# Optimization experiments

Hardware: AMD Instinct MI355X
Metric: run time of the kernel (lower is better)

Reference implementation:

```python
import jax, jax.numpy as jnp
import numpy as np


def setup_inputs() -> dict:
    key = jax.random.key(0)
    k1, k2 = jax.random.split(key)
    B, T, D, K = 16, 800, 256, 64
    x = jax.random.normal(k1, (B, T, D), dtype=jnp.float32)
    mu = jax.random.normal(k2, (K, D), dtype=jnp.float32)
    prec = jnp.ones((K,), dtype=jnp.float32)
    return {"x": x, "mu": mu, "prec": prec}


def reference(x, mu, prec):
    # x: (B,T,D), mu: (K,D), prec: (K,)
    delta = x[:, :, None, :] - mu[None, None, :, :]          # (B,T,K,D)
    dist = jnp.sum(delta * delta, axis=-1)                   # (B,T,K) dist_pow=2
    llk = -(prec * prec) * dist                              # use_bias=False -> bias=0
    r = jax.nn.softmax(llk, axis=-1)                         # softmax over components K
    r = r / (jnp.sum(r, axis=1, keepdims=True) + 1e-9)       # normalize over time T
    pool = jnp.einsum('btk,btkd->bkd', r, delta)             # weighted sum over T
    return pool.reshape(x.shape[0], -1)                      # (B, K*D)
```

## Files before the change

kernel.cpp:

```cpp
#include <hip/hip_runtime.h>

#define B_ 16
#define T_ 800
#define D_ 256
#define K_ 64
#define NTILE 13

__global__ __launch_bounds__(512, 1) void kernelAB(
    const float* __restrict__ x, const float* __restrict__ mu,
    const float* __restrict__ prec, float* __restrict__ Pp, float* __restrict__ Spart)
{
    __shared__ float xs[64 * 260];
    __shared__ float mus[64 * 260];
    __shared__ float rt[64 * 68];
    __shared__ float xxs[64];
    __shared__ float mms[64];
    __shared__ float sred[8][64];

    const int tid  = threadIdx.x;
    const int tx   = tid >> 4;
    const int ky   = tid & 15;
    const int b    = blockIdx.x / NTILE;
    const int tile = blockIdx.x % NTILE;
    const int t0   = tile * 64;

    #pragma unroll
    for (int jj = 0; jj < 8; ++jj) {
        const int g   = tid + jj * 512;
        const int row = g >> 6, col = g & 63;
        int trow = t0 + row; if (trow > T_ - 1) trow = T_ - 1;
        *(float4*)&xs[row * 260 + col * 4] =
            *(const float4*)(x + ((size_t)(b * T_ + trow)) * D_ + col * 4);
        *(float4*)&mus[row * 260 + col * 4] =
            *(const float4*)(mu + (size_t)row * D_ + col * 4);
    }
    __syncthreads();

    {
        const int srow = tid >> 3, sq = tid & 7;
        float xxp = 0.f, mmp = 0.f;
        #pragma unroll
        for (int m = 0; m < 8; ++m) {
            float4 v = *(const float4*)&xs[srow * 260 + (sq * 8 + m) * 4];
            xxp = fmaf(v.x, v.x, xxp); xxp = fmaf(v.y, v.y, xxp);
            xxp = fmaf(v.z, v.z, xxp); xxp = fmaf(v.w, v.w, xxp);
            float4 u = *(const float4*)&mus[srow * 260 + (sq * 8 + m) * 4];
            mmp = fmaf(u.x, u.x, mmp); mmp = fmaf(u.y, u.y, mmp);
            mmp = fmaf(u.z, u.z, mmp); mmp = fmaf(u.w, u.w, mmp);
        }
        xxp += __shfl_xor(xxp, 1); xxp += __shfl_xor(xxp, 2); xxp += __shfl_xor(xxp, 4);
        mmp += __shfl_xor(mmp, 1); mmp += __shfl_xor(mmp, 2); mmp += __shfl_xor(mmp, 4);
        if (sq == 0) { xxs[srow] = xxp; mms[srow] = mmp; }
    }
    __syncthreads();

    float acc[2][4];
    #pragma unroll
    for (int i = 0; i < 2; ++i)
        #pragma unroll
        for (int j = 0; j < 4; ++j) acc[i][j] = 0.f;

    #pragma unroll 4
    for (int dg = 0; dg < 64; ++dg) {
        float4 xv[2], mv[4];
        #pragma unroll
        for (int i = 0; i < 2; ++i) xv[i] = *(const float4*)&xs[(tx * 2 + i) * 260 + dg * 4];
        #pragma unroll
        for (int j = 0; j < 4; ++j) mv[j] = *(const float4*)&mus[(ky + 16 * j) * 260 + dg * 4];
        #pragma unroll
        for (int i = 0; i < 2; ++i)
            #pragma unroll
            for (int j = 0; j < 4; ++j) {
                float a = acc[i][j];
                a = fmaf(xv[i].x, mv[j].x, a);
                a = fmaf(xv[i].y, mv[j].y, a);
                a = fmaf(xv[i].z, mv[j].z, a);
                a = fmaf(xv[i].w, mv[j].w, a);
                acc[i][j] = a;
            }
    }

    float p2[4], mmk[4];
    #pragma unroll
    for (int j = 0; j < 4; ++j) {
        float p = prec[ky + 16 * j];
        p2[j] = p * p;
        mmk[j] = mms[ky + 16 * j];
    }

    float sacc[4] = {0.f, 0.f, 0.f, 0.f};
    #pragma unroll
    for (int i = 0; i < 2; ++i) {
        const int tl = tx * 2 + i;
        const bool valid = (t0 + tl) < T_;
        const float xxv = xxs[tl];
        float llk[4];
        #pragma unroll
        for (int j = 0; j < 4; ++j)
            llk[j] = p2[j] * (2.f * acc[i][j] - xxv - mmk[j]);
        float mx = fmaxf(fmaxf(llk[0], llk[1]), fmaxf(llk[2], llk[3]));
        mx = fmaxf(mx, __shfl_xor(mx, 1)); mx = fmaxf(mx, __shfl_xor(mx, 2));
        mx = fmaxf(mx, __shfl_xor(mx, 4)); mx = fmaxf(mx, __shfl_xor(mx, 8));
        float e[4], ps = 0.f;
        #pragma unroll
        for (int j = 0; j < 4; ++j) { e[j] = __expf(llk[j] - mx); ps += e[j]; }
        ps += __shfl_xor(ps, 1); ps += __shfl_xor(ps, 2);
        ps += __shfl_xor(ps, 4); ps += __shfl_xor(ps, 8);
        const float inv = valid ? (1.f / ps) : 0.f;
        float4 rv;
        rv.x = e[0] * inv; rv.y = e[1] * inv; rv.z = e[2] * inv; rv.w = e[3] * inv;
        *(float4*)&rt[tl * 68 + ky * 4] = rv;
        sacc[0] += rv.x; sacc[1] += rv.y; sacc[2] += rv.z; sacc[3] += rv.w;
    }

    #pragma unroll
    for (int j = 0; j < 4; ++j) {
        sacc[j] += __shfl_xor(sacc[j], 16);
        sacc[j] += __shfl_xor(sacc[j], 32);
    }
    const int w = tid >> 6;
    if ((tid & 48) == 0) {
        #pragma unroll
        for (int j = 0; j < 4; ++j) sred[w][ky * 4 + j] = sacc[j];
    }
    __syncthreads();
    if (tid < 64) {
        const int k = tid;
        const int slot = (k & 15) * 4 + (k >> 4);
        float s = 0.f;
        #pragma unroll
        for (int q = 0; q < 8; ++q) s += sred[q][slot];
        Spart[((size_t)b * NTILE + tile) * K_ + k] = s;
    }

    const int dhalf = tid & 31;
    const int kx2   = tid >> 5;

    float4 pa[4][2];
    #pragma unroll
    for (int j = 0; j < 4; ++j) {
        pa[j][0] = make_float4(0.f, 0.f, 0.f, 0.f);
        pa[j][1] = make_float4(0.f, 0.f, 0.f, 0.f);
    }

    #pragma unroll 8
    for (int tt = 0; tt < 64; ++tt) {
        const float4 rv  = *(const float4*)&rt[tt * 68 + kx2 * 4];
        const float4 xv0 = *(const float4*)&xs[tt * 260 + dhalf * 4];
        const float4 xv1 = *(const float4*)&xs[tt * 260 + 128 + dhalf * 4];
        #pragma unroll
        for (int j = 0; j < 4; ++j) {
            const float rj = (j == 0) ? rv.x : (j == 1) ? rv.y : (j == 2) ? rv.z : rv.w;
            pa[j][0].x = fmaf(rj, xv0.x, pa[j][0].x);
            pa[j][0].y = fmaf(rj, xv0.y, pa[j][0].y);
            pa[j][0].z = fmaf(rj, xv0.z, pa[j][0].z);
            pa[j][0].w = fmaf(rj, xv0.w, pa[j][0].w);
            pa[j][1].x = fmaf(rj, xv1.x, pa[j][1].x);
            pa[j][1].y = fmaf(rj, xv1.y, pa[j][1].y);
            pa[j][1].z = fmaf(rj, xv1.z, pa[j][1].z);
            pa[j][1].w = fmaf(rj, xv1.w, pa[j][1].w);
        }
    }

    float* Pb = Pp + ((size_t)(b * NTILE + tile)) * K_ * D_;
    #pragma unroll
    for (int j = 0; j < 4; ++j) {
        const int k = kx2 + 16 * j;
        float* dst = Pb + (size_t)k * D_ + dhalf * 4;
        *(float4*)(dst)       = pa[j][0];
        *(float4*)(dst + 128) = pa[j][1];
    }
}

__global__ __launch_bounds__(256) void kernelC(
    const float* __restrict__ Pp, const float* __restrict__ Spart,
    const float* __restrict__ mu, float* __restrict__ out)
{
    const int o4 = blockIdx.x * 256 + threadIdx.x;
    const int d4 = o4 & 63;
    const int k  = (o4 >> 6) & 63;
    const int b  = o4 >> 12;

    float s = 0.f;
    #pragma unroll
    for (int p = 0; p < NTILE; ++p)
        s += Spart[((size_t)b * NTILE + p) * K_ + k];

    float4 acc = make_float4(0.f, 0.f, 0.f, 0.f);
    #pragma unroll
    for (int p = 0; p < NTILE; ++p) {
        float4 v = ((const float4*)Pp)[((size_t)(b * NTILE + p) * K_ + k) * (D_ / 4) + d4];
        acc.x += v.x; acc.y += v.y; acc.z += v.z; acc.w += v.w;
    }
    const float inv = 1.f / (s + 1e-9f);
    const float sm  = s * inv;
    const float4 m = ((const float4*)mu)[k * 64 + d4];
    float4 o;
    o.x = acc.x * inv - sm * m.x;
    o.y = acc.y * inv - sm * m.y;
    o.z = acc.z * inv - sm * m.z;
    o.w = acc.w * inv - sm * m.w;
    ((float4*)out)[o4] = o;
}

extern "C" void kernel_launch(void* const* d_in, const int* in_sizes, int n_in,
                              void* d_out, int out_size, void* d_ws, size_t ws_size,
                              hipStream_t stream) {
    const float* x    = (const float*)d_in[0];
    const float* mu   = (const float*)d_in[1];
    const float* prec = (const float*)d_in[2];
    float* out = (float*)d_out;

    float* Pp    = (float*)d_ws;
    float* Spart = Pp + (size_t)B_ * NTILE * K_ * D_;

    kernelAB<<<B_ * NTILE, 512, 0, stream>>>(x, mu, prec, Pp, Spart);
    kernelC<<<256, 256, 0, stream>>>(Pp, Spart, mu, out);
}
```

Measured before the change: 85.01 us.

## Use split-bf16 MFMA for distance and pooling GEMMs, precompute norms in prep kernel

Both matmuls in kernelAB (x·mu for distances and r^T·x for pooling) move from scalar FP32 FMAs to bf16 MFMA 16x16x32 instructions. fp32 precision is emulated by splitting operands into hi/lo bf16 parts: three products for the distance GEMM, and for pooling the responsibilities are rounded to bf16 while x keeps its hi/lo split. A new prep kernel precomputes the squared norms of x and mu and prec^2 in global memory. The block shrinks to 256 threads, and x is transposed into an XOR-swizzled shared layout for the second GEMM. This adds an extra launch and a full read of x, and the bf16 rounding of r may cost accuracy.

```diff
diff --git a/kernel.cpp b/kernel.cpp
--- a/kernel.cpp
+++ b/kernel.cpp
@@ -6,169 +6,213 @@
 #define K_ 64
 #define NTILE 13
 
-__global__ __launch_bounds__(512, 1) void kernelAB(
+typedef __attribute__((ext_vector_type(8))) short short8v;
+typedef __attribute__((ext_vector_type(4))) float f32x4v;
+
+__device__ __forceinline__ ushort bf16rn(float v) {
+    unsigned int b = __float_as_uint(v);
+    return (ushort)((b + 0x7fffu + ((b >> 16) & 1u)) >> 16);
+}
+__device__ __forceinline__ float bf16hi(ushort h) {
+    return __uint_as_float(((unsigned int)h) << 16);
+}
+
+__global__ __launch_bounds__(256) void prep(
+    const float* __restrict__ x, const float* __restrict__ mu, const float* __restrict__ prec,
+    float* __restrict__ xx_g, float* __restrict__ mm_g, float* __restrict__ p2_g)
+{
+    const int bid = blockIdx.x, tid = threadIdx.x;
+    if (bid < 3200) {
+        const int row = bid * 4 + (tid >> 6), lane = tid & 63;
+        float4 v = ((const float4*)x)[(size_t)row * 64 + lane];
+        float s = v.x*v.x + v.y*v.y + v.z*v.z + v.w*v.w;
+        #pragma unroll
+        for (int off = 32; off > 0; off >>= 1) s += __shfl_xor(s, off);
+        if (lane == 0) xx_g[row] = s;
+    } else if (bid < 3216) {
+        const int row = (bid - 3200) * 4 + (tid >> 6), lane = tid & 63;
+        float4 v = ((const float4*)mu)[(size_t)row * 64 + lane];
+        float s = v.x*v.x + v.y*v.y + v.z*v.z + v.w*v.w;
+        #pragma unroll
+        for (int off = 32; off > 0; off >>= 1) s += __shfl_xor(s, off);
+        if (lane == 0) mm_g[row] = s;
+    } else {
+        if (tid < 64) { float p = prec[tid]; p2_g[tid] = p * p; }
+    }
+}
+
+__global__ __launch_bounds__(256, 1) void kernelAB(
     const float* __restrict__ x, const float* __restrict__ mu,
-    const float* __restrict__ prec, float* __restrict__ Pp, float* __restrict__ Spart)
+    const float* __restrict__ xx_g, const float* __restrict__ mm_g,
+    const float* __restrict__ p2_g,
+    float* __restrict__ Pp, float* __restrict__ Spart)
 {
-    __shared__ float xs[64 * 260];
-    __shared__ float mus[64 * 260];
-    __shared__ float rt[64 * 68];
-    __shared__ float xxs[64];
-    __shared__ float mms[64];
-    __shared__ float sred[8][64];
+    __shared__ ushort xh_s[64 * 264];
+    __shared__ ushort xl_s[64 * 264];
+    __shared__ ushort muh_s[64 * 264];
+    __shared__ ushort mul_s[64 * 264];
+    __shared__ ushort rtT_s[64 * 72];
+    __shared__ float xxs[64], mms[64], p2s[64];
+    __shared__ float sred[4][64];
 
     const int tid  = threadIdx.x;
-    const int tx   = tid >> 4;
-    const int ky   = tid & 15;
+    const int lane = tid & 63;
+    const int w    = tid >> 6;
+    const int m    = lane & 15;
+    const int q    = lane >> 4;
     const int b    = blockIdx.x / NTILE;
     const int tile = blockIdx.x % NTILE;
     const int t0   = tile * 64;
 
-    #pragma unroll
-    for (int jj = 0; jj < 8; ++jj) {
-        const int g   = tid + jj * 512;
-        const int row = g >> 6, col = g & 63;
+    if (tid < 64)       xxs[tid]       = xx_g[b * T_ + min(t0 + tid, T_ - 1)];
+    else if (tid < 128) mms[tid - 64]  = mm_g[tid - 64];
+    else if (tid < 192) p2s[tid - 128] = p2_g[tid - 128];
+
+    #pragma unroll 4
+    for (int jj = 0; jj < 16; ++jj) {
+        const int idx = tid + jj * 256;
+        const int row = idx >> 6, c = idx & 63;
         int trow = t0 + row; if (trow > T_ - 1) trow = T_ - 1;
-        *(float4*)&xs[row * 260 + col * 4] =
-            *(const float4*)(x + ((size_t)(b * T_ + trow)) * D_ + col * 4);
-        *(float4*)&mus[row * 260 + col * 4] =
-            *(const float4*)(mu + (size_t)row * D_ + col * 4);
+        float4 v = ((const float4*)x)[(size_t)(b * T_ + trow) * 64 + c];
+        ushort4 h, l;
+        h.x = bf16rn(v.x); l.x = bf16rn(v.x - bf16hi(h.x));
+        h.y = bf16rn(v.y); l.y = bf16rn(v.y - bf16hi(h.y));
+        h.z = bf16rn(v.z); l.z = bf16rn(v.z - bf16hi(h.z));
+        h.w = bf16rn(v.w); l.w = bf16rn(v.w - bf16hi(h.w));
+        *(ushort4*)&xh_s[row * 264 + c * 4] = h;
+        *(ushort4*)&xl_s[row * 264 + c * 4] = l;
+    }
+    #pragma unroll 4
+    for (int jj = 0; jj < 16; ++jj) {
+        const int idx = tid + jj * 256;
+        const int row = idx >> 6, c = idx & 63;
+        float4 v = ((const float4*)mu)[(size_t)row * 64 + c];
+        ushort4 h, l;
+        h.x = bf16rn(v.x); l.x = bf16rn(v.x - bf16hi(h.x));
+        h.y = bf16rn(v.y); l.y = bf16rn(v.y - bf16hi(h.y));
+        h.z = bf16rn(v.z); l.z = bf16rn(v.z - bf16hi(h.z));
+        h.w = bf16rn(v.w); l.w = bf16rn(v.w - bf16hi(h.w));
+        *(ushort4*)&muh_s[row * 264 + c * 4] = h;
+        *(ushort4*)&mul_s[row * 264 + c * 4] = l;
     }
     __syncthreads();
 
-    {
-        const int srow = tid >> 3, sq = tid & 7;
-        float xxp = 0.f, mmp = 0.f;
-        #pragma unroll
-        for (int m = 0; m < 8; ++m) {
-            float4 v = *(const float4*)&xs[srow * 260 + (sq * 8 + m) * 4];
-            xxp = fmaf(v.x, v.x, xxp); xxp = fmaf(v.y, v.y, xxp);
-            xxp = fmaf(v.z, v.z, xxp); xxp = fmaf(v.w, v.w, xxp);
-            float4 u = *(const float4*)&mus[srow * 260 + (sq * 8 + m) * 4];
-            mmp = fmaf(u.x, u.x, mmp); mmp = fmaf(u.y, u.y, mmp);
-            mmp = fmaf(u.z, u.z, mmp); mmp = fmaf(u.w, u.w, mmp);
-        }
-        xxp += __shfl_xor(xxp, 1); xxp += __shfl_xor(xxp, 2); xxp += __shfl_xor(xxp, 4);
-        mmp += __shfl_xor(mmp, 1); mmp += __shfl_xor(mmp, 2); mmp += __shfl_xor(mmp, 4);
-        if (sq == 0) { xxs[srow] = xxp; mms[srow] = mmp; }
-    }
-    __syncthreads();
-
-    float acc[2][4];
-    #pragma unroll
-    for (int i = 0; i < 2; ++i)
-        #pragma unroll
-        for (int j = 0; j < 4; ++j) acc[i][j] = 0.f;
-
-    #pragma unroll 4
-    for (int dg = 0; dg < 64; ++dg) {
-        float4 xv[2], mv[4];
-        #pragma unroll
-        for (int i = 0; i < 2; ++i) xv[i] = *(const float4*)&xs[(tx * 2 + i) * 260 + dg * 4];
-        #pragma unroll
-        for (int j = 0; j < 4; ++j) mv[j] = *(const float4*)&mus[(ky + 16 * j) * 260 + dg * 4];
-        #pragma unroll
-        for (int i = 0; i < 2; ++i)
-            #pragma unroll
-            for (int j = 0; j < 4; ++j) {
-                float a = acc[i][j];
-                a = fmaf(xv[i].x, mv[j].x, a);
-                a = fmaf(xv[i].y, mv[j].y, a);
-                a = fmaf(xv[i].z, mv[j].z, a);
-                a = fmaf(xv[i].w, mv[j].w, a);
-                acc[i][j] = a;
-            }
-    }
-
-    float p2[4], mmk[4];
-    #pragma unroll
-    for (int j = 0; j < 4; ++j) {
-        float p = prec[ky + 16 * j];
-        p2[j] = p * p;
-        mmk[j] = mms[ky + 16 * j];
-    }
-
+    f32x4v acc[4];
+    #pragma unroll
+    for (int nt = 0; nt < 4; ++nt) acc[nt] = (f32x4v){0.f, 0.f, 0.f, 0.f};
+
+    #pragma unroll 2
+    for (int c = 0; c < 8; ++c) {
+        const int ao = (w * 16 + m) * 264 + c * 32 + q * 8;
+        short8v ah = *(const short8v*)&xh_s[ao];
+        short8v al = *(const short8v*)&xl_s[ao];
+        #pragma unroll
+        for (int nt = 0; nt < 4; ++nt) {
+            const int bo = (nt * 16 + m) * 264 + c * 32 + q * 8;
+            short8v bh = *(const short8v*)&muh_s[bo];
+            short8v bl = *(const short8v*)&mul_s[bo];
+            acc[nt] = __builtin_amdgcn_mfma_f32_16x16x32_bf16(ah, bh, acc[nt], 0, 0, 0);
+            acc[nt] = __builtin_amdgcn_mfma_f32_16x16x32_bf16(ah, bl, acc[nt], 0, 0, 0);
+            acc[nt] = __builtin_amdgcn_mfma_f32_16x16x32_bf16(al, bh, acc[nt], 0, 0, 0);
+        }
+    }
+
+    float mmk[4], p2k[4];
+    #pragma unroll
+    for (int nt = 0; nt < 4; ++nt) { mmk[nt] = mms[nt * 16 + m]; p2k[nt] = p2s[nt * 16 + m]; }
+
+    ushort4 rp[4];
     float sacc[4] = {0.f, 0.f, 0.f, 0.f};
     #pragma unroll
-    for (int i = 0; i < 2; ++i) {
-        const int tl = tx * 2 + i;
+    for (int r = 0; r < 4; ++r) {
+        const int tl = w * 16 + q * 4 + r;
+        const float xxv = xxs[tl];
         const bool valid = (t0 + tl) < T_;
-        const float xxv = xxs[tl];
         float llk[4];
         #pragma unroll
-        for (int j = 0; j < 4; ++j)
-            llk[j] = p2[j] * (2.f * acc[i][j] - xxv - mmk[j]);
+        for (int nt = 0; nt < 4; ++nt)
+            llk[nt] = p2k[nt] * (2.f * acc[nt][r] - xxv - mmk[nt]);
         float mx = fmaxf(fmaxf(llk[0], llk[1]), fmaxf(llk[2], llk[3]));
         mx = fmaxf(mx, __shfl_xor(mx, 1)); mx = fmaxf(mx, __shfl_xor(mx, 2));
         mx = fmaxf(mx, __shfl_xor(mx, 4)); mx = fmaxf(mx, __shfl_xor(mx, 8));
         float e[4], ps = 0.f;
         #pragma unroll
-        for (int j = 0; j < 4; ++j) { e[j] = __expf(llk[j] - mx); ps += e[j]; }
+        for (int nt = 0; nt < 4; ++nt) { e[nt] = __expf(llk[nt] - mx); ps += e[nt]; }
         ps += __shfl_xor(ps, 1); ps += __shfl_xor(ps, 2);
         ps += __shfl_xor(ps, 4); ps += __shfl_xor(ps, 8);
         const float inv = valid ? (1.f / ps) : 0.f;
-        float4 rv;
-        rv.x = e[0] * inv; rv.y = e[1] * inv; rv.z = e[2] * inv; rv.w = e[3] * inv;
-        *(float4*)&rt[tl * 68 + ky * 4] = rv;
-        sacc[0] += rv.x; sacc[1] += rv.y; sacc[2] += rv.z; sacc[3] += rv.w;
-    }
-
-    #pragma unroll
-    for (int j = 0; j < 4; ++j) {
-        sacc[j] += __shfl_xor(sacc[j], 16);
-        sacc[j] += __shfl_xor(sacc[j], 32);
-    }
-    const int w = tid >> 6;
-    if ((tid & 48) == 0) {
-        #pragma unroll
-        for (int j = 0; j < 4; ++j) sred[w][ky * 4 + j] = sacc[j];
+        #pragma unroll
+        for (int nt = 0; nt < 4; ++nt) {
+            float rv = e[nt] * inv;
+            sacc[nt] += rv;
+            ((ushort*)&rp[nt])[r] = bf16rn(rv);
+        }
+    }
+    #pragma unroll
+    for (int nt = 0; nt < 4; ++nt)
+        *(ushort4*)&rtT_s[(nt * 16 + m) * 72 + w * 16 + q * 4] = rp[nt];
+    #pragma unroll
+    for (int nt = 0; nt < 4; ++nt) {
+        sacc[nt] += __shfl_xor(sacc[nt], 16);
+        sacc[nt] += __shfl_xor(sacc[nt], 32);
+    }
+    if (q == 0) {
+        #pragma unroll
+        for (int nt = 0; nt < 4; ++nt) sred[w][nt * 16 + m] = sacc[nt];
     }
     __syncthreads();
+
     if (tid < 64) {
-        const int k = tid;
-        const int slot = (k & 15) * 4 + (k >> 4);
-        float s = 0.f;
-        #pragma unroll
-        for (int q = 0; q < 8; ++q) s += sred[q][slot];
-        Spart[((size_t)b * NTILE + tile) * K_ + k] = s;
-    }
-
-    const int dhalf = tid & 31;
-    const int kx2   = tid >> 5;
-
-    float4 pa[4][2];
-    #pragma unroll
-    for (int j = 0; j < 4; ++j) {
-        pa[j][0] = make_float4(0.f, 0.f, 0.f, 0.f);
-        pa[j][1] = make_float4(0.f, 0.f, 0.f, 0.f);
-    }
-
-    #pragma unroll 8
-    for (int tt = 0; tt < 64; ++tt) {
-        const float4 rv  = *(const float4*)&rt[tt * 68 + kx2 * 4];
-        const float4 xv0 = *(const float4*)&xs[tt * 260 + dhalf * 4];
-        const float4 xv1 = *(const float4*)&xs[tt * 260 + 128 + dhalf * 4];
-        #pragma unroll
-        for (int j = 0; j < 4; ++j) {
-            const float rj = (j == 0) ? rv.x : (j == 1) ? rv.y : (j == 2) ? rv.z : rv.w;
-            pa[j][0].x = fmaf(rj, xv0.x, pa[j][0].x);
-            pa[j][0].y = fmaf(rj, xv0.y, pa[j][0].y);
-            pa[j][0].z = fmaf(rj, xv0.z, pa[j][0].z);
-            pa[j][0].w = fmaf(rj, xv0.w, pa[j][0].w);
-            pa[j][1].x = fmaf(rj, xv1.x, pa[j][1].x);
-            pa[j][1].y = fmaf(rj, xv1.y, pa[j][1].y);
-            pa[j][1].z = fmaf(rj, xv1.z, pa[j][1].z);
-            pa[j][1].w = fmaf(rj, xv1.w, pa[j][1].w);
+        float s = sred[0][tid] + sred[1][tid] + sred[2][tid] + sred[3][tid];
+        Spart[((size_t)b * NTILE + tile) * K_ + tid] = s;
+    }
+
+    {
+        const int tp = tid & 31, dg = tid >> 5;
+        #pragma unroll
+        for (int c = 0; c < 4; ++c) {
+            short8v a0 = *(const short8v*)&xh_s[(2 * tp)     * 264 + dg * 32 + c * 8];
+            short8v a1 = *(const short8v*)&xh_s[(2 * tp + 1) * 264 + dg * 32 + c * 8];
+            short8v b0 = *(const short8v*)&xl_s[(2 * tp)     * 264 + dg * 32 + c * 8];
+            short8v b1 = *(const short8v*)&xl_s[(2 * tp + 1) * 264 + dg * 32 + c * 8];
+            #pragma unroll
+            for (int j = 0; j < 8; ++j) {
+                const int d = dg * 32 + c * 8 + j;
+                const int widx = (tp & 3) + 4 * ((tp >> 2) ^ (d & 7));
+                ushort2 hv, lv;
+                hv.x = (ushort)a0[j]; hv.y = (ushort)a1[j];
+                lv.x = (ushort)b0[j]; lv.y = (ushort)b1[j];
+                *(ushort2*)&muh_s[d * 64 + widx * 2] = hv;
+                *(ushort2*)&mul_s[d * 64 + widx * 2] = lv;
+            }
+        }
+    }
+    __syncthreads();
+
+    f32x4v acc2[16];
+    #pragma unroll
+    for (int nt = 0; nt < 16; ++nt) acc2[nt] = (f32x4v){0.f, 0.f, 0.f, 0.f};
+
+    #pragma unroll
+    for (int tc = 0; tc < 2; ++tc) {
+        short8v ar = *(const short8v*)&rtT_s[(w * 16 + m) * 72 + tc * 32 + q * 8];
+        #pragma unroll
+        for (int nt = 0; nt < 16; ++nt) {
+            const int drow = nt * 16 + m;
+            const int eoff = ((tc * 4 + q) ^ (drow & 7)) * 8;
+            short8v bh = *(const short8v*)&muh_s[drow * 64 + eoff];
+            short8v bl = *(const short8v*)&mul_s[drow * 64 + eoff];
+            acc2[nt] = __builtin_amdgcn_mfma_f32_16x16x32_bf16(ar, bh, acc2[nt], 0, 0, 0);
+            acc2[nt] = __builtin_amdgcn_mfma_f32_16x16x32_bf16(ar, bl, acc2[nt], 0, 0, 0);
         }
     }
 
     float* Pb = Pp + ((size_t)(b * NTILE + tile)) * K_ * D_;
     #pragma unroll
-    for (int j = 0; j < 4; ++j) {
-        const int k = kx2 + 16 * j;
-        float* dst = Pb + (size_t)k * D_ + dhalf * 4;
-        *(float4*)(dst)       = pa[j][0];
-        *(float4*)(dst + 128) = pa[j][1];
+    for (int nt = 0; nt < 16; ++nt) {
+        #pragma unroll
+        for (int r = 0; r < 4; ++r)
+            Pb[(size_t)(w * 16 + q * 4 + r) * D_ + nt * 16 + m] = acc2[nt][r];
     }
 }
 
@@ -213,7 +257,11 @@
 
     float* Pp    = (float*)d_ws;
     float* Spart = Pp + (size_t)B_ * NTILE * K_ * D_;
-
-    kernelAB<<<B_ * NTILE, 512, 0, stream>>>(x, mu, prec, Pp, Spart);
+    float* xx_g  = Spart + (size_t)B_ * NTILE * K_;
+    float* mm_g  = xx_g + (size_t)B_ * T_;
+    float* p2_g  = mm_g + 64;
+
+    prep<<<3217, 256, 0, stream>>>(x, mu, prec, xx_g, mm_g, p2_g);
+    kernelAB<<<B_ * NTILE, 256, 0, stream>>>(x, mu, xx_g, mm_g, p2_g, Pp, Spart);
     kernelC<<<256, 256, 0, stream>>>(Pp, Spart, mu, out);
 }
```

Measured after the change: 80.27 us. 5.6% less time.
